# Kernel tuning notes

Measured on AMD Instinct MI355X. Metric: run time of the kernel, lower is better.

Reference implementation:

```python
import jax, jax.numpy as jnp
import numpy as np

HEADS = 8
DIM_HEAD = 64

def setup_inputs() -> dict:
    key = jax.random.key(0)
    ks = jax.random.split(key, 9)
    B, N1, N2, D = 4, 2048, 2048, 1024
    inner = HEADS * DIM_HEAD  # 512
    s_in = 1.0 / np.sqrt(D)
    s_inner = 1.0 / np.sqrt(inner)
    return {
        "x1": jax.random.normal(ks[0], (B, N1, D), jnp.float32),
        "x2": jax.random.normal(ks[1], (B, N2, D), jnp.float32),
        "Wq1": jax.random.normal(ks[2], (D, inner), jnp.float32) * s_in,
        "Wk1": jax.random.normal(ks[3], (D, inner), jnp.float32) * s_in,
        "Wv1": jax.random.normal(ks[4], (D, inner), jnp.float32) * s_in,
        "Wk2": jax.random.normal(ks[5], (D, inner), jnp.float32) * s_in,
        "Wv2": jax.random.normal(ks[6], (D, inner), jnp.float32) * s_in,
        "Wo": jax.random.normal(ks[7], (inner, D), jnp.float32) * s_inner,
        "bo": jnp.zeros((D,), jnp.float32),
    }

def reference(x1, x2, Wq1, Wk1, Wv1, Wk2, Wv2, Wo, bo):
    h, d = HEADS, DIM_HEAD
    scale = d ** (-0.5)
    B, N1, _ = x1.shape
    N2 = x2.shape[1]

    def split_heads(t, n):
        return t.reshape(B, n, h, d)  # [B, n, h, d]

    q1 = split_heads(x1 @ Wq1, N1)
    k1 = split_heads(x1 @ Wk1, N1)
    v1 = split_heads(x1 @ Wv1, N1)
    k2 = split_heads(x2 @ Wk2, N2)
    v2 = split_heads(x2 @ Wv2, N2)

    k = jnp.concatenate([k1, k2], axis=1)  # [B, N1+N2, h, d]
    v = jnp.concatenate([v1, v2], axis=1)

    # fp32 precision for QK^T (matches _ATTN_PRECISION == 'fp32')
    sim = jnp.einsum('bihd,bjhd->bhij', q1.astype(jnp.float32),
                     k.astype(jnp.float32)) * scale  # [B, h, N1, N1+N2]
    attn = jax.nn.softmax(sim, axis=-1)
    out = jnp.einsum('bhij,bjhd->bihd', attn, v)  # [B, N1, h, d]
    out = out.reshape(B, N1, h * d)
    return out @ Wo + bo
```

## Files before the change

kernel.cpp:

```cpp
#include <hip/hip_runtime.h>
#include <stdint.h>

typedef __bf16 bf16x8 __attribute__((ext_vector_type(8)));
typedef float f32x4 __attribute__((ext_vector_type(4)));
typedef unsigned short ushort_t;

#define MFMA16(a,b,c) __builtin_amdgcn_mfma_f32_16x16x32_bf16((a),(b),(c),0,0,0)

__device__ __forceinline__ unsigned short f2bf(float f){
    unsigned u = __builtin_bit_cast(unsigned, f);
    u += 0x7fffu + ((u>>16)&1u);
    return (unsigned short)(u>>16);
}
__device__ __forceinline__ unsigned pack2bf(float lo, float hi){
    unsigned a = __builtin_bit_cast(unsigned, lo) + 0x8000u;
    unsigned b = __builtin_bit_cast(unsigned, hi) + 0x8000u;
    return __builtin_amdgcn_perm(b, a, 0x07060302u);
}
__device__ __forceinline__ float fexp2(float x){
#if __has_builtin(__builtin_amdgcn_exp2f)
    return __builtin_amdgcn_exp2f(x);
#else
    return exp2f(x);
#endif
}

__device__ __forceinline__ void async16(ushort_t* lds, const ushort_t* g){
#if __has_builtin(__builtin_amdgcn_global_load_lds)
    __builtin_amdgcn_global_load_lds(
        (const __attribute__((address_space(1))) void*)g,
        (__attribute__((address_space(3))) void*)lds, 16, 0, 0);
#else
    const int l = (int)(threadIdx.x & 63u);
    *(uint4*)(lds + (size_t)l*8) = *(const uint4*)g;
#endif
}

__global__ __launch_bounds__(256) void convert_x(const float* __restrict__ src,
                                                 ushort_t* __restrict__ dst){
    size_t i = ((size_t)blockIdx.x*256 + threadIdx.x)*8;
    float4 a = *(const float4*)(src + i);
    float4 b = *(const float4*)(src + i + 4);
    uint4 o;
    o.x = pack2bf(a.x, a.y); o.y = pack2bf(a.z, a.w);
    o.z = pack2bf(b.x, b.y); o.w = pack2bf(b.z, b.w);
    *(uint4*)(dst + i) = o;
}

__global__ __launch_bounds__(256) void transpose_w(
    const float* __restrict__ w0, const float* __restrict__ w1,
    const float* __restrict__ w2, const float* __restrict__ w3,
    const float* __restrict__ w4,
    ushort_t* __restrict__ Wt1, ushort_t* __restrict__ Wt2)
{
    int z = blockIdx.z;
    const float* src; ushort_t* dst;
    if (z < 3)  { src = (z==0)?w0:((z==1)?w1:w2); dst = Wt1 + (size_t)z*512*1024; }
    else        { src = (z==3)?w3:w4;             dst = Wt2 + (size_t)(z-3)*512*1024; }
    const int N = 512;
    int k0 = blockIdx.x*32, n0 = blockIdx.y*32;
    __shared__ float T[32][33];
    int t = threadIdx.x;
    int kr = t>>3, nc = (t&7)*4;
    float4 v = *(const float4*)(src + (size_t)(k0+kr)*N + n0 + nc);
    T[kr][nc] = v.x; T[kr][nc+1] = v.y; T[kr][nc+2] = v.z; T[kr][nc+3] = v.w;
    __syncthreads();
    int nr = t>>3, kc = (t&7)*4;
    uint2 o;
    o.x = pack2bf(T[kc][nr],   T[kc+1][nr]);
    o.y = pack2bf(T[kc+2][nr], T[kc+3][nr]);
    *(uint2*)(dst + (size_t)(n0+nr)*1024 + k0 + kc) = o;
}

__global__ __launch_bounds__(256) void transpose_wo(
    const float* __restrict__ src, ushort_t* __restrict__ dst)
{
    __shared__ float T[64][33];
    const int k0 = blockIdx.x*64;
    const int n0 = blockIdx.y*32;
    const int t = threadIdx.x;
    const int kr = t>>3, nc = (t&7)*4;
#pragma unroll
    for (int hf = 0; hf < 2; ++hf){
        float4 v = *(const float4*)(src + (size_t)(k0 + hf*32 + kr)*1024 + n0 + nc);
        T[hf*32+kr][nc]   = v.x; T[hf*32+kr][nc+1] = v.y;
        T[hf*32+kr][nc+2] = v.z; T[hf*32+kr][nc+3] = v.w;
    }
    __syncthreads();
    const int nr = t>>3, kc = (t&7)*8;
    ushort_t tmp[8];
#pragma unroll
    for (int e = 0; e < 8; ++e){
        int dp = kc + e;
        int d  = ((dp&3)<<4) | (dp>>2);
        tmp[e] = f2bf(T[d][nr]);
    }
    *(uint4*)(dst + (size_t)(n0+nr)*512 + k0 + kc) = *(uint4*)tmp;
}

__global__ __launch_bounds__(256) void proj_fused(
    const ushort_t* __restrict__ X1, const ushort_t* __restrict__ X2,
    const ushort_t* __restrict__ W1, const ushort_t* __restrict__ W2,
    ushort_t* __restrict__ Qp, ushort_t* __restrict__ Kp, ushort_t* __restrict__ Vtp)
{
    __shared__ ushort_t As[2][128][32];
    __shared__ ushort_t Bs[2][128][32];
    const int t = threadIdx.x;
    const int m0 = blockIdx.x*128;
    const int y  = blockIdx.y;
    const ushort_t* A; const ushort_t* Bt; int n0, koff, sub;
    if (y < 12) { A = X1; Bt = W1; n0 = y*128;      koff = 0;    sub = n0>>9; }
    else        { A = X2; Bt = W2; n0 = (y-12)*128; koff = 2048; sub = 1 + (n0>>9); }

    const int w = t>>6, l = t&63;
    const int quad = l>>4, lc = l&15;
    const int wr = (w>>1)*64, wc = (w&1)*64;
    const int KD = 1024;

    f32x4 acc[4][4] = {};

    const int crow = l>>2;
    const int kseg = (l&3)*8;
    const ushort_t* gA0 = A  + (size_t)(m0 + w*32      + crow)*KD + kseg;
    const ushort_t* gA1 = A  + (size_t)(m0 + w*32 + 16 + crow)*KD + kseg;
    const ushort_t* gB0 = Bt + (size_t)(n0 + w*32      + crow)*KD + kseg;
    const ushort_t* gB1 = Bt + (size_t)(n0 + w*32 + 16 + crow)*KD + kseg;

    async16(&As[0][w*32][0],    gA0);
    async16(&As[0][w*32+16][0], gA1);
    async16(&Bs[0][w*32][0],    gB0);
    async16(&Bs[0][w*32+16][0], gB1);
    __syncthreads();

    for (int kk = 0; kk < 32; ++kk) {
        const int cur = kk & 1;
        if (kk + 1 < 32) {
            const int k0 = (kk+1)*32;
            const int nx = cur ^ 1;
            async16(&As[nx][w*32][0],    gA0 + k0);
            async16(&As[nx][w*32+16][0], gA1 + k0);
            async16(&Bs[nx][w*32][0],    gB0 + k0);
            async16(&Bs[nx][w*32+16][0], gB1 + k0);
        }
        bf16x8 af[4], bfv[4];
#pragma unroll
        for (int i = 0; i < 4; ++i) {
            af[i]  = *(const bf16x8*)&As[cur][wr + i*16 + lc][quad*8];
            bfv[i] = *(const bf16x8*)&Bs[cur][wc + i*16 + lc][quad*8];
        }
#pragma unroll
        for (int mt = 0; mt < 4; ++mt)
#pragma unroll
            for (int nt = 0; nt < 4; ++nt)
                acc[mt][nt] = MFMA16(af[mt], bfv[nt], acc[mt][nt]);
        __syncthreads();
    }

    const int hh = ((n0 + wc)>>6) & 7;
    const int dp = 4*lc;
    const float QSC = 0.18033688011112042f;
    if (sub == 0) {
#pragma unroll
        for (int mt = 0; mt < 4; ++mt) {
            const int row = m0 + wr + mt*16 + quad*4;
            const int b = row>>11, i = row & 2047;
#pragma unroll
            for (int r = 0; r < 4; ++r) {
                uint2 o;
                o.x = pack2bf(acc[mt][0][r]*QSC, acc[mt][1][r]*QSC);
                o.y = pack2bf(acc[mt][2][r]*QSC, acc[mt][3][r]*QSC);
                *(uint2*)(Qp + ((size_t)(b*8+hh)*2048 + i + r)*64 + dp) = o;
            }
        }
    } else if (sub == 1) {
#pragma unroll
        for (int mt = 0; mt < 4; ++mt) {
            const int row = m0 + wr + mt*16 + quad*4;
            const int b = row>>11, i = row & 2047;
#pragma unroll
            for (int r = 0; r < 4; ++r) {
                uint2 o;
                o.x = pack2bf(acc[mt][0][r], acc[mt][1][r]);
                o.y = pack2bf(acc[mt][2][r], acc[mt][3][r]);
                *(uint2*)(Kp + ((size_t)(b*8+hh)*4096 + koff + i + r)*64 + dp) = o;
            }
        }
    } else {
#pragma unroll
        for (int mt = 0; mt < 4; ++mt) {
            const int row = m0 + wr + mt*16 + quad*4;
            const int b = row>>11, i = row & 2047;
            const int tile = (koff + i) >> 6;
            const int slot = 32*(mt>>1) + 4*(mt&1) + 8*quad;
#pragma unroll
            for (int nt = 0; nt < 4; ++nt) {
                uint2 o;
                o.x = pack2bf(acc[mt][nt][0], acc[mt][nt][1]);
                o.y = pack2bf(acc[mt][nt][2], acc[mt][nt][3]);
                *(uint2*)(Vtp + (((size_t)(b*8+hh)*64 + tile)*64 + dp + nt)*64 + slot) = o;
            }
        }
    }
}

__global__ __launch_bounds__(256) void out_gemm(
    const ushort_t* __restrict__ A, const ushort_t* __restrict__ Bt,
    float* __restrict__ outF, const float* __restrict__ bias)
{
    __shared__ ushort_t As[2][128][32];
    __shared__ ushort_t Bs[2][128][32];
    const int t = threadIdx.x;
    const int m0 = blockIdx.x*128, n0 = blockIdx.y*128;
    const int w = t>>6, l = t&63;
    const int quad = l>>4, lc = l&15;
    const int wr = (w>>1)*64, wc = (w&1)*64;
    const int KD = 512;

    f32x4 acc[4][4] = {};

    const int crow = l>>2;
    const int kseg = (l&3)*8;
    const ushort_t* gA0 = A  + (size_t)(m0 + w*32      + crow)*KD + kseg;
    const ushort_t* gA1 = A  + (size_t)(m0 + w*32 + 16 + crow)*KD + kseg;
    const ushort_t* gB0 = Bt + (size_t)(n0 + w*32      + crow)*KD + kseg;
    const ushort_t* gB1 = Bt + (size_t)(n0 + w*32 + 16 + crow)*KD + kseg;

    async16(&As[0][w*32][0],    gA0);
    async16(&As[0][w*32+16][0], gA1);
    async16(&Bs[0][w*32][0],    gB0);
    async16(&Bs[0][w*32+16][0], gB1);
    __syncthreads();

    for (int kk = 0; kk < 16; ++kk) {
        const int cur = kk & 1;
        if (kk + 1 < 16) {
            const int k0 = (kk+1)*32;
            const int nx = cur ^ 1;
            async16(&As[nx][w*32][0],    gA0 + k0);
            async16(&As[nx][w*32+16][0], gA1 + k0);
            async16(&Bs[nx][w*32][0],    gB0 + k0);
            async16(&Bs[nx][w*32+16][0], gB1 + k0);
        }
        bf16x8 af[4], bfv[4];
#pragma unroll
        for (int i = 0; i < 4; ++i) {
            af[i]  = *(const bf16x8*)&As[cur][wr + i*16 + lc][quad*8];
            bfv[i] = *(const bf16x8*)&Bs[cur][wc + i*16 + lc][quad*8];
        }
#pragma unroll
        for (int mt = 0; mt < 4; ++mt)
#pragma unroll
            for (int nt = 0; nt < 4; ++nt)
                acc[mt][nt] = MFMA16(af[mt], bfv[nt], acc[mt][nt]);
        __syncthreads();
    }

    float bv[4];
#pragma unroll
    for (int nt = 0; nt < 4; ++nt) bv[nt] = bias[n0 + wc + nt*16 + lc];
#pragma unroll
    for (int mt = 0; mt < 4; ++mt) {
        const int row = m0 + wr + mt*16 + quad*4;
#pragma unroll
        for (int nt = 0; nt < 4; ++nt) {
            const int col = n0 + wc + nt*16 + lc;
#pragma unroll
            for (int r = 0; r < 4; ++r)
                outF[(size_t)(row+r)*1024 + col] = acc[mt][nt][r] + bv[nt];
        }
    }
}

__global__ __launch_bounds__(256) void flash_attn(
    const ushort_t* __restrict__ Q, const ushort_t* __restrict__ Kg,
    const ushort_t* __restrict__ Vt,
    float* __restrict__ O0, float* __restrict__ O1, float* __restrict__ Lp)
{
    __shared__ ushort_t Ks[2][64][72];
    __shared__ ushort_t Vs[2][64][72];
    const int bh = blockIdx.x, qt = blockIdx.y, z = blockIdx.z;
    const int b = bh>>3, h = bh&7;
    const int t = threadIdx.x, wv = t>>6, l = t&63;
    const int quad = l>>4, lc = l&15;

    const ushort_t* qbase = Q + ((size_t)bh*2048 + qt*128 + wv*16 + lc)*64;
    bf16x8 qA0 = *(const bf16x8*)(qbase + quad*8);
    bf16x8 qA1 = *(const bf16x8*)(qbase + 32 + quad*8);
    bf16x8 qB0 = *(const bf16x8*)(qbase + 64*64 + quad*8);
    bf16x8 qB1 = *(const bf16x8*)(qbase + 64*64 + 32 + quad*8);

    const ushort_t* Kb = Kg + ((size_t)bh*4096 + (size_t)z*2048)*64;
    const ushort_t* Vb = Vt + ((size_t)bh*4096 + (size_t)z*2048)*64;

    const int srow = t>>2, sseg = (t&3)*16;
    const ushort_t* kst = Kb + (size_t)t*16;
    const ushort_t* vst = Vb + (size_t)t*16;

    float l0 = 0.0f, l1 = 0.0f;
    f32x4 o0[4] = {}, o1[4] = {};

    uint4 ka  = *(const uint4*)(kst);
    uint4 kb2 = *(const uint4*)(kst + 8);
    uint4 va  = *(const uint4*)(vst);
    uint4 vb2 = *(const uint4*)(vst + 8);

    for (int jt = 0; jt < 32; ++jt) {
        const int cur = jt & 1;
        ushort_t* ksd = &Ks[cur][srow][sseg];
        ushort_t* vsd = &Vs[cur][srow][sseg];
        *(uint4*)ksd     = ka;
        *(uint4*)(ksd+8) = kb2;
        *(uint4*)vsd     = va;
        *(uint4*)(vsd+8) = vb2;
        __syncthreads();
        if (jt < 31) {
            const size_t j0 = (size_t)(jt+1)*4096;
            ka  = *(const uint4*)(kst + j0);
            kb2 = *(const uint4*)(kst + j0 + 8);
            va  = *(const uint4*)(vst + j0);
            vb2 = *(const uint4*)(vst + j0 + 8);
        }

        f32x4 s0[4], s1[4];
#pragma unroll
        for (int kt = 0; kt < 4; ++kt) {
            bf16x8 kf0 = *(const bf16x8*)&Ks[cur][kt*16 + lc][quad*8];
            bf16x8 kf1 = *(const bf16x8*)&Ks[cur][kt*16 + lc][32 + quad*8];
            f32x4 z0 = {}, z1 = {};
            z0 = MFMA16(kf0, qA0, z0); z0 = MFMA16(kf1, qA1, z0);
            z1 = MFMA16(kf0, qB0, z1); z1 = MFMA16(kf1, qB1, z1);
            s0[kt] = z0; s1[kt] = z1;
        }

        union { unsigned u[8]; bf16x8 v[2]; } p0, p1;
        float rs0 = 0.0f, rs1 = 0.0f;
#pragma unroll
        for (int kt = 0; kt < 4; ++kt) {
            float a0 = fexp2(s0[kt][0]), a1v = fexp2(s0[kt][1]);
            float a2 = fexp2(s0[kt][2]), a3 = fexp2(s0[kt][3]);
            rs0 += (a0 + a1v) + (a2 + a3);
            p0.u[kt*2]   = pack2bf(a0, a1v);
            p0.u[kt*2+1] = pack2bf(a2, a3);
            float c0 = fexp2(s1[kt][0]), c1 = fexp2(s1[kt][1]);
            float c2 = fexp2(s1[kt][2]), c3 = fexp2(s1[kt][3]);
            rs1 += (c0 + c1) + (c2 + c3);
            p1.u[kt*2]   = pack2bf(c0, c1);
            p1.u[kt*2+1] = pack2bf(c2, c3);
        }
        l0 += rs0; l1 += rs1;

#pragma unroll
        for (int dt = 0; dt < 4; ++dt) {
            bf16x8 vf0 = *(const bf16x8*)&Vs[cur][dt*16 + lc][quad*8];
            bf16x8 vf1 = *(const bf16x8*)&Vs[cur][dt*16 + lc][32 + quad*8];
            o0[dt] = MFMA16(vf0, p0.v[0], o0[dt]);
            o0[dt] = MFMA16(vf1, p0.v[1], o0[dt]);
            o1[dt] = MFMA16(vf0, p1.v[0], o1[dt]);
            o1[dt] = MFMA16(vf1, p1.v[1], o1[dt]);
        }
    }

    l0 += __shfl_xor(l0, 16); l0 += __shfl_xor(l0, 32);
    l1 += __shfl_xor(l1, 16); l1 += __shfl_xor(l1, 32);

    float* OP = z ? O1 : O0;
    const int qgA = qt*128 + wv*16 + lc;
    size_t baseA = ((size_t)b*2048 + qgA)*512 + h*64 + quad*4;
    size_t baseB = baseA + (size_t)64*512;
#pragma unroll
    for (int dt = 0; dt < 4; ++dt) {
        *(f32x4*)(OP + baseA + dt*16) = o0[dt];
        *(f32x4*)(OP + baseB + dt*16) = o1[dt];
    }
    if (quad == 0) {
        Lp[(size_t)z*65536 + bh*2048 + qgA]      = l0;
        Lp[(size_t)z*65536 + bh*2048 + qgA + 64] = l1;
    }
}

__global__ __launch_bounds__(256) void reduce_o(
    const float* __restrict__ O0, const float* __restrict__ O1,
    const float* __restrict__ Lp, ushort_t* __restrict__ AO)
{
    size_t i = ((size_t)blockIdx.x*256 + threadIdx.x)*4;
    int row = (int)(i >> 9);
    int col = (int)(i & 511);
    int b = row >> 11, q = row & 2047, h = col >> 6;
    size_t li = (size_t)(b*8 + h)*2048 + q;
    float lsum = Lp[li] + Lp[65536 + li];
    float linv = 1.0f / lsum;
    float4 a = *(const float4*)(O0 + i);
    float4 c = *(const float4*)(O1 + i);
    uint2 o;
    o.x = pack2bf((a.x + c.x)*linv, (a.y + c.y)*linv);
    o.y = pack2bf((a.z + c.z)*linv, (a.w + c.w)*linv);
    *(uint2*)(AO + i) = o;
}

extern "C" void kernel_launch(void* const* d_in, const int* in_sizes, int n_in,
                              void* d_out, int out_size, void* d_ws, size_t ws_size,
                              hipStream_t stream)
{
    const float* x1  = (const float*)d_in[0];
    const float* x2  = (const float*)d_in[1];
    const float* Wq1 = (const float*)d_in[2];
    const float* Wk1 = (const float*)d_in[3];
    const float* Wv1 = (const float*)d_in[4];
    const float* Wk2 = (const float*)d_in[5];
    const float* Wv2 = (const float*)d_in[6];
    const float* Wo  = (const float*)d_in[7];
    const float* bo  = (const float*)d_in[8];
    float* out = (float*)d_out;

    ushort_t* ws  = (ushort_t*)d_ws;
    ushort_t* Xc1 = ws;
    ushort_t* Xc2 = Xc1 + 8388608;
    ushort_t* Wt1 = Xc2 + 8388608;
    ushort_t* Wt2 = Wt1 + 1572864;
    ushort_t* Wot = Wt2 + 1048576;
    ushort_t* Qp  = Wot + 524288;
    ushort_t* Kp  = Qp  + 4194304;
    ushort_t* Vtp = Kp  + 8388608;

    float* Opart0 = (float*)Xc1;
    float* Opart1 = (float*)Xc2;
    float* Lp     = (float*)Wt1;
    ushort_t* AOp = Qp;

    convert_x<<<4096, 256, 0, stream>>>(x1, Xc1);
    convert_x<<<4096, 256, 0, stream>>>(x2, Xc2);
    transpose_w<<<dim3(32,16,5), 256, 0, stream>>>(Wq1,Wk1,Wv1,Wk2,Wv2, Wt1,Wt2);
    transpose_wo<<<dim3(8,32), 256, 0, stream>>>(Wo, Wot);

    proj_fused<<<dim3(64,20), 256, 0, stream>>>(Xc1, Xc2, Wt1, Wt2, Qp, Kp, Vtp);

    flash_attn<<<dim3(32,16,2), 256, 0, stream>>>(Qp, Kp, Vtp, Opart0, Opart1, Lp);

    reduce_o<<<4096, 256, 0, stream>>>(Opart0, Opart1, Lp, AOp);

    out_gemm<<<dim3(64,8), 256, 0, stream>>>(AOp, Wot, out, bo);
}
```

Baseline: 297.8 us.

## Stream K/V tiles into LDS with async global-to-LDS loads and XOR swizzle

Replaces the register-staged K/V prefetch, where tiles were loaded into registers and then written to padded shared memory, with direct async global-to-LDS copies into double buffers. An XOR swizzle replaces the row padding to avoid bank conflicts. The single barrier moves to the end of each iteration. Row sums are now kept as vector partials and reduced after the loop. This frees registers and removes the LDS store instructions, but correctness depends on the async16 helper (defined elsewhere) completing before the barrier, i.e. on proper vmcnt waits.

```diff
diff --git a/kernel.cpp b/kernel.cpp
--- a/kernel.cpp
+++ b/kernel.cpp
@@ -276,8 +276,8 @@
     const ushort_t* __restrict__ Vt,
     float* __restrict__ O0, float* __restrict__ O1, float* __restrict__ Lp)
 {
-    __shared__ ushort_t Ks[2][64][72];
-    __shared__ ushort_t Vs[2][64][72];
+    __shared__ ushort_t KsF[2*4096];
+    __shared__ ushort_t VsF[2*4096];
     const int bh = blockIdx.x, qt = blockIdx.y, z = blockIdx.z;
     const int b = bh>>3, h = bh&7;
     const int t = threadIdx.x, wv = t>>6, l = t&63;
@@ -289,43 +289,44 @@
     bf16x8 qB0 = *(const bf16x8*)(qbase + 64*64 + quad*8);
     bf16x8 qB1 = *(const bf16x8*)(qbase + 64*64 + 32 + quad*8);
 
-    const ushort_t* Kb = Kg + ((size_t)bh*4096 + (size_t)z*2048)*64;
-    const ushort_t* Vb = Vt + ((size_t)bh*4096 + (size_t)z*2048)*64;
-
-    const int srow = t>>2, sseg = (t&3)*16;
-    const ushort_t* kst = Kb + (size_t)t*16;
-    const ushort_t* vst = Vb + (size_t)t*16;
-
-    float l0 = 0.0f, l1 = 0.0f;
+    const size_t kvoff = ((size_t)bh*4096 + (size_t)z*2048)*64;
+    const int lb = (l>>3)*64 + (((l&7) ^ ((l>>3)&7))*8);
+    const ushort_t* gK = Kg + kvoff + lb + wv*1024;
+    const ushort_t* gV = Vt + kvoff + lb + wv*1024;
+    ushort_t* ldsK = KsF + wv*1024;
+    ushort_t* ldsV = VsF + wv*1024;
+
+    const int colA = (quad ^ (lc&7))*8;
+    const int colB = colA ^ 32;
+
+    f32x4 ls0 = {}, ls1 = {};
     f32x4 o0[4] = {}, o1[4] = {};
 
-    uint4 ka  = *(const uint4*)(kst);
-    uint4 kb2 = *(const uint4*)(kst + 8);
-    uint4 va  = *(const uint4*)(vst);
-    uint4 vb2 = *(const uint4*)(vst + 8);
+    async16(ldsK,       gK);
+    async16(ldsK + 512, gK + 512);
+    async16(ldsV,       gV);
+    async16(ldsV + 512, gV + 512);
+    __syncthreads();
 
     for (int jt = 0; jt < 32; ++jt) {
         const int cur = jt & 1;
-        ushort_t* ksd = &Ks[cur][srow][sseg];
-        ushort_t* vsd = &Vs[cur][srow][sseg];
-        *(uint4*)ksd     = ka;
-        *(uint4*)(ksd+8) = kb2;
-        *(uint4*)vsd     = va;
-        *(uint4*)(vsd+8) = vb2;
-        __syncthreads();
+        const int curo = cur*4096;
         if (jt < 31) {
-            const size_t j0 = (size_t)(jt+1)*4096;
-            ka  = *(const uint4*)(kst + j0);
-            kb2 = *(const uint4*)(kst + j0 + 8);
-            va  = *(const uint4*)(vst + j0);
-            vb2 = *(const uint4*)(vst + j0 + 8);
+            const int nxo = (cur^1)*4096;
+            const ushort_t* gk = gK + (size_t)(jt+1)*4096;
+            const ushort_t* gv = gV + (size_t)(jt+1)*4096;
+            async16(ldsK + nxo,       gk);
+            async16(ldsK + nxo + 512, gk + 512);
+            async16(ldsV + nxo,       gv);
+            async16(ldsV + nxo + 512, gv + 512);
         }
 
         f32x4 s0[4], s1[4];
 #pragma unroll
         for (int kt = 0; kt < 4; ++kt) {
-            bf16x8 kf0 = *(const bf16x8*)&Ks[cur][kt*16 + lc][quad*8];
-            bf16x8 kf1 = *(const bf16x8*)&Ks[cur][kt*16 + lc][32 + quad*8];
+            const ushort_t* kr = KsF + curo + (kt*16 + lc)*64;
+            bf16x8 kf0 = *(const bf16x8*)(kr + colA);
+            bf16x8 kf1 = *(const bf16x8*)(kr + colB);
             f32x4 z0 = {}, z1 = {};
             z0 = MFMA16(kf0, qA0, z0); z0 = MFMA16(kf1, qA1, z0);
             z1 = MFMA16(kf0, qB0, z1); z1 = MFMA16(kf1, qB1, z1);
@@ -333,33 +334,36 @@
         }
 
         union { unsigned u[8]; bf16x8 v[2]; } p0, p1;
-        float rs0 = 0.0f, rs1 = 0.0f;
 #pragma unroll
         for (int kt = 0; kt < 4; ++kt) {
-            float a0 = fexp2(s0[kt][0]), a1v = fexp2(s0[kt][1]);
-            float a2 = fexp2(s0[kt][2]), a3 = fexp2(s0[kt][3]);
-            rs0 += (a0 + a1v) + (a2 + a3);
-            p0.u[kt*2]   = pack2bf(a0, a1v);
-            p0.u[kt*2+1] = pack2bf(a2, a3);
-            float c0 = fexp2(s1[kt][0]), c1 = fexp2(s1[kt][1]);
-            float c2 = fexp2(s1[kt][2]), c3 = fexp2(s1[kt][3]);
-            rs1 += (c0 + c1) + (c2 + c3);
-            p1.u[kt*2]   = pack2bf(c0, c1);
-            p1.u[kt*2+1] = pack2bf(c2, c3);
-        }
-        l0 += rs0; l1 += rs1;
+            f32x4 e0, e1;
+            e0[0] = fexp2(s0[kt][0]); e0[1] = fexp2(s0[kt][1]);
+            e0[2] = fexp2(s0[kt][2]); e0[3] = fexp2(s0[kt][3]);
+            ls0 += e0;
+            p0.u[kt*2]   = pack2bf(e0[0], e0[1]);
+            p0.u[kt*2+1] = pack2bf(e0[2], e0[3]);
+            e1[0] = fexp2(s1[kt][0]); e1[1] = fexp2(s1[kt][1]);
+            e1[2] = fexp2(s1[kt][2]); e1[3] = fexp2(s1[kt][3]);
+            ls1 += e1;
+            p1.u[kt*2]   = pack2bf(e1[0], e1[1]);
+            p1.u[kt*2+1] = pack2bf(e1[2], e1[3]);
+        }
 
 #pragma unroll
         for (int dt = 0; dt < 4; ++dt) {
-            bf16x8 vf0 = *(const bf16x8*)&Vs[cur][dt*16 + lc][quad*8];
-            bf16x8 vf1 = *(const bf16x8*)&Vs[cur][dt*16 + lc][32 + quad*8];
+            const ushort_t* vr = VsF + curo + (dt*16 + lc)*64;
+            bf16x8 vf0 = *(const bf16x8*)(vr + colA);
+            bf16x8 vf1 = *(const bf16x8*)(vr + colB);
             o0[dt] = MFMA16(vf0, p0.v[0], o0[dt]);
             o0[dt] = MFMA16(vf1, p0.v[1], o0[dt]);
             o1[dt] = MFMA16(vf0, p1.v[0], o1[dt]);
             o1[dt] = MFMA16(vf1, p1.v[1], o1[dt]);
         }
-    }
-
+        __syncthreads();
+    }
+
+    float l0 = (ls0[0] + ls0[1]) + (ls0[2] + ls0[3]);
+    float l1 = (ls1[0] + ls1[1]) + (ls1[2] + ls1[3]);
     l0 += __shfl_xor(l0, 16); l0 += __shfl_xor(l0, 32);
     l1 += __shfl_xor(l1, 16); l1 += __shfl_xor(l1, 32);
 
```

Measured after the change: 299.9 us. No clear change (+0.7%).
